# Kernel tuning notes

Hardware: AMD Instinct MI355X
Metric: run time of the kernel (lower is better)

Reference implementation:

```python
import jax, jax.numpy as jnp
import numpy as np

EPS = 1e-12  # F.normalize default eps (denominator = max(norm, eps))


def setup_inputs() -> dict:
    key = jax.random.key(0)
    ks = jax.random.split(key, 8)
    B, FIN, H, W = 4, 256, 64, 64
    N_MEM, SQ = 64, 16           # sqrt_fin = fin**0.5
    POS_CH = 2                    # PosEncoding concatenates one coord channel per dim
    CIN = FIN + POS_CH
    QK = N_MEM * SQ               # 1024
    # PosEncoding buffer: normalized coordinate grid in [-1, 1], shape [2, H, W]
    ys = jnp.linspace(-1.0, 1.0, H, dtype=jnp.float32)
    xs = jnp.linspace(-1.0, 1.0, W, dtype=jnp.float32)
    gy, gx = jnp.meshgrid(ys, xs, indexing='ij')
    pos = jnp.stack([gy, gx], axis=0)
    s = 0.02
    return {
        'x':    jax.random.normal(ks[0], (B, FIN, H, W), jnp.float32),
        'pos':  pos,
        'wq':   jax.random.normal(ks[1], (QK, CIN), jnp.float32) * s,
        'bq':   jnp.zeros((QK,), jnp.float32),
        'wk':   jax.random.normal(ks[2], (QK, CIN), jnp.float32) * s,
        'bk':   jnp.zeros((QK,), jnp.float32),
        'v':    jax.random.normal(ks[3], (N_MEM, FIN), jnp.float32) * s,
        'wout': jax.random.normal(ks[4], (FIN, FIN), jnp.float32) * s,
        'bout': jnp.zeros((FIN,), jnp.float32),
    }


def reference(x, pos, wq, bq, wk, bk, v, wout, bout):
    B, C, H, W = x.shape
    S = H * W
    n_mem, fin = v.shape
    sq = wq.shape[0] // n_mem
    # PosEncoding: concat coordinate channels
    posb = jnp.broadcast_to(pos[None], (B,) + pos.shape)
    xp = jnp.concatenate([x, posb], axis=1).reshape(B, C + pos.shape[0], S)
    # 1x1 conv projections (channel GEMMs)
    q = jnp.einsum('oc,bcs->bos', wq, xp) + bq[None, :, None]  # [B, n_mem*sq, S]
    k = jnp.einsum('oc,bcs->bos', wk, xp) + bk[None, :, None]
    q = q.reshape(B, n_mem, sq, S).transpose(0, 3, 1, 2)  # [B,S,m,sq]
    k = k.reshape(B, n_mem, sq, S).transpose(0, 3, 2, 1)  # [B,S,sq,m]
    # F.normalize: q over last dim (sqrt_fin), k over dim=1 (sqrt_fin)
    qn = q / jnp.maximum(jnp.linalg.norm(q, axis=-1, keepdims=True), EPS)
    kn = k / jnp.maximum(jnp.linalg.norm(k, axis=2, keepdims=True), EPS)
    # attn[b,s,m,n] = qn . kn ; dropout is identity in eval mode.
    # mean over memory slots m commutes with (attn @ v), so fuse:
    attn_mean = jnp.einsum('bsk,bskn->bsn', qn.mean(axis=2), kn)  # [B,S,n_mem]
    mem = attn_mean @ v                                            # [B,S,fin]
    mem = mem.transpose(0, 2, 1).reshape(B, fin, H, W)
    out = jnp.einsum('of,bfhw->bohw', wout, mem) + bout[None, :, None, None]
    return x + out
```

## Files before the change

kernel.cpp:

```cpp
#include <hip/hip_runtime.h>
#include <stdint.h>

#define EPSN 1e-12f

typedef float f32x4 __attribute__((ext_vector_type(4)));
typedef __bf16 bf16x8 __attribute__((ext_vector_type(8)));

__device__ __forceinline__ unsigned short f2bf(float f) {
  union { float f; unsigned int u; } v; v.f = f;
  unsigned int u = v.u + 0x7FFFu + ((v.u >> 16) & 1u);
  return (unsigned short)(u >> 16);
}

#define WQP_OFF 0
#define WKP_OFF (1024 * 288)
#define WVP_OFF (2 * 1024 * 288)

__global__ __launch_bounds__(256) void prep_kernel(
    const float* __restrict__ wq, const float* __restrict__ bq,
    const float* __restrict__ wk, const float* __restrict__ bk,
    const float* __restrict__ v, const float* __restrict__ wout,
    unsigned short* __restrict__ wsp) {
  int idx = blockIdx.x * 256 + threadIdx.x;
  if (idx < 1024 * 288) {
    int o = idx / 288, k = idx - o * 288;
    float vq, vk;
    if (k < 258)      { vq = wq[o * 258 + k]; vk = wk[o * 258 + k]; }
    else if (k == 258){ vq = bq[o];           vk = bk[o]; }
    else              { vq = 0.f;             vk = 0.f; }
    wsp[WQP_OFF + idx] = f2bf(vq);
    wsp[WKP_OFF + idx] = f2bf(vk);
  }
  if (idx < 256 * 64) {
    int o = idx >> 6, m = idx & 63;
    const float* wo = wout + o * 256;
    const float* vm = v + m * 256;
    float s = 0.f;
    for (int f = 0; f < 256; ++f) s = fmaf(wo[f], vm[f], s);
    wsp[WVP_OFF + idx] = f2bf(s);
  }
}

#define KP 296

__global__ __launch_bounds__(1024) void fused_kernel(
    const float* __restrict__ x, const float* __restrict__ pos,
    const unsigned short* __restrict__ wsp, const float* __restrict__ bout,
    float* __restrict__ out) {
  __shared__ __align__(16) unsigned short xp[64 * KP];
  __shared__ __align__(16) float qbarL[16 * 66];
  __shared__ __align__(16) unsigned short attnT[64 * 72];
  __shared__ float boutL[256];

  const int tid = threadIdx.x;
  const int lane = tid & 63;
  const int wid = __builtin_amdgcn_readfirstlane(tid >> 6);
  const int col = lane & 15, quad = lane >> 4;
  const int P0 = blockIdx.x * 64;
  const int b = P0 >> 12, s0 = P0 & 4095;

  for (int i = tid; i < 64 * KP; i += 1024) {
    int c = i >> 6, p = i & 63;
    float vv;
    if (c < 256)        vv = x[(b * 256 + c) * 4096 + s0 + p];
    else if (c < 258)   vv = pos[(c - 256) * 4096 + s0 + p];
    else if (c == 258)  vv = 1.0f;
    else                vv = 0.0f;
    xp[p * KP + c] = f2bf(vv);
  }
  if (tid < 256) boutL[tid] = bout[tid];
  for (int i = tid; i < 16 * 66; i += 1024) qbarL[i] = 0.f;
  __syncthreads();

  f32x4 acc[4][4];
#pragma unroll
  for (int ot = 0; ot < 4; ++ot)
#pragma unroll
    for (int nt = 0; nt < 4; ++nt) acc[ot][nt] = (f32x4)0.f;

  {
    const unsigned short* wbase = wsp + WQP_OFF + (wid * 64 + col) * 288 + quad * 8;
#pragma unroll 1
    for (int ks = 0; ks < 9; ++ks) {
      const int kb = ks * 32;
      bf16x8 av[4], bv[4];
#pragma unroll
      for (int ot = 0; ot < 4; ++ot)
        av[ot] = *(const bf16x8*)(wbase + ot * 16 * 288 + kb);
#pragma unroll
      for (int nt = 0; nt < 4; ++nt)
        bv[nt] = *(const bf16x8*)(&xp[(nt * 16 + col) * KP + kb + quad * 8]);
#pragma unroll
      for (int ot = 0; ot < 4; ++ot)
#pragma unroll
        for (int nt = 0; nt < 4; ++nt)
          acc[ot][nt] = __builtin_amdgcn_mfma_f32_16x16x32_bf16(av[ot], bv[nt], acc[ot][nt], 0, 0, 0);
    }
  }

  {
    float qsum[4][4];
#pragma unroll
    for (int nt = 0; nt < 4; ++nt)
#pragma unroll
      for (int r = 0; r < 4; ++r) qsum[nt][r] = 0.f;
#pragma unroll
    for (int ot = 0; ot < 4; ++ot) {
#pragma unroll
      for (int nt = 0; nt < 4; ++nt) {
        f32x4 a = acc[ot][nt];
        float s = a[0]*a[0] + a[1]*a[1] + a[2]*a[2] + a[3]*a[3];
        s += __shfl_xor(s, 16, 64);
        s += __shfl_xor(s, 32, 64);
        float inv = 1.0f / fmaxf(sqrtf(s), EPSN);
#pragma unroll
        for (int r = 0; r < 4; ++r) qsum[nt][r] = fmaf(a[r], inv, qsum[nt][r]);
      }
    }
#pragma unroll
    for (int nt = 0; nt < 4; ++nt)
#pragma unroll
      for (int r = 0; r < 4; ++r)
        atomicAdd(&qbarL[(quad * 4 + r) * 66 + nt * 16 + col], qsum[nt][r] * (1.0f / 64.0f));
  }
  __syncthreads();

#pragma unroll
  for (int ot = 0; ot < 4; ++ot)
#pragma unroll
    for (int nt = 0; nt < 4; ++nt) acc[ot][nt] = (f32x4)0.f;

  {
    const unsigned short* wbase = wsp + WKP_OFF + (wid * 64 + col) * 288 + quad * 8;
#pragma unroll 1
    for (int ks = 0; ks < 9; ++ks) {
      const int kb = ks * 32;
      bf16x8 av[4], bv[4];
#pragma unroll
      for (int ot = 0; ot < 4; ++ot)
        av[ot] = *(const bf16x8*)(wbase + ot * 16 * 288 + kb);
#pragma unroll
      for (int nt = 0; nt < 4; ++nt)
        bv[nt] = *(const bf16x8*)(&xp[(nt * 16 + col) * KP + kb + quad * 8]);
#pragma unroll
      for (int ot = 0; ot < 4; ++ot)
#pragma unroll
        for (int nt = 0; nt < 4; ++nt)
          acc[ot][nt] = __builtin_amdgcn_mfma_f32_16x16x32_bf16(av[ot], bv[nt], acc[ot][nt], 0, 0, 0);
    }
  }

  {
    float qb[4][4];
#pragma unroll
    for (int nt = 0; nt < 4; ++nt)
#pragma unroll
      for (int r = 0; r < 4; ++r)
        qb[nt][r] = qbarL[(quad * 4 + r) * 66 + nt * 16 + col];

#pragma unroll
    for (int ot = 0; ot < 4; ++ot) {
      const int m = wid * 4 + ot;
#pragma unroll
      for (int nt = 0; nt < 4; ++nt) {
        f32x4 a = acc[ot][nt];
        float s2 = a[0]*a[0] + a[1]*a[1] + a[2]*a[2] + a[3]*a[3];
        float sp = qb[nt][0]*a[0] + qb[nt][1]*a[1] + qb[nt][2]*a[2] + qb[nt][3]*a[3];
        s2 += __shfl_xor(s2, 16, 64);
        s2 += __shfl_xor(s2, 32, 64);
        sp += __shfl_xor(sp, 16, 64);
        sp += __shfl_xor(sp, 32, 64);
        float attn = sp / fmaxf(sqrtf(s2), EPSN);
        if (quad == 0) attnT[(nt * 16 + col) * 72 + m] = f2bf(attn);
      }
    }
  }
  __syncthreads();

  {
    f32x4 e[4];
#pragma unroll
    for (int nt = 0; nt < 4; ++nt) e[nt] = (f32x4)0.f;
    const unsigned short* wvb = wsp + WVP_OFF + (wid * 16 + col) * 64 + quad * 8;
#pragma unroll
    for (int ks = 0; ks < 2; ++ks) {
      bf16x8 av = *(const bf16x8*)(wvb + ks * 32);
#pragma unroll
      for (int nt = 0; nt < 4; ++nt) {
        bf16x8 bv = *(const bf16x8*)(&attnT[(nt * 16 + col) * 72 + ks * 32 + quad * 8]);
        e[nt] = __builtin_amdgcn_mfma_f32_16x16x32_bf16(av, bv, e[nt], 0, 0, 0);
      }
    }
#pragma unroll
    for (int nt = 0; nt < 4; ++nt) {
#pragma unroll
      for (int r = 0; r < 4; ++r) {
        const int o = wid * 16 + quad * 4 + r;
        const int p = nt * 16 + col;
        const int gi = (b * 256 + o) * 4096 + s0 + p;
        out[gi] = x[gi] + boutL[o] + e[nt][r];
      }
    }
  }
}

extern "C" void kernel_launch(void* const* d_in, const int* in_sizes, int n_in,
                              void* d_out, int out_size, void* d_ws, size_t ws_size,
                              hipStream_t stream) {
  const float* x    = (const float*)d_in[0];
  const float* pos  = (const float*)d_in[1];
  const float* wq   = (const float*)d_in[2];
  const float* bq   = (const float*)d_in[3];
  const float* wk   = (const float*)d_in[4];
  const float* bk   = (const float*)d_in[5];
  const float* v    = (const float*)d_in[6];
  const float* wout = (const float*)d_in[7];
  const float* bout = (const float*)d_in[8];
  float* out = (float*)d_out;
  unsigned short* wsp = (unsigned short*)d_ws;

  hipLaunchKernelGGL(prep_kernel, dim3(1152), dim3(256), 0, stream,
                     wq, bq, wk, bk, v, wout, wsp);
  hipLaunchKernelGGL(fused_kernel, dim3(256), dim3(1024), 0, stream,
                     x, pos, wsp, bout, out);
}
```

Baseline: 150.5 us.

## Pre-swizzle Q/K weights into MFMA fragment order and vectorize prep and staging

The prep kernel now writes the Q and K weights in MFMA fragment order, so each lane's 8-element bf16 A-operand sits contiguous and the wave's loads coalesce into one 1KB block. The K-loop over the weights is fully unrolled. The Wout·V product is split four ways per output with shuffle reduction and vector loads. The x-to-LDS staging packs two bf16 channels per 32-bit store. Together these target the strided global weight loads, the slow serial prep dot-products, and LDS store count, at the cost of more register pressure from unrolling.

```diff
diff --git a/kernel.cpp b/kernel.cpp
--- a/kernel.cpp
+++ b/kernel.cpp
@@ -5,6 +5,7 @@
 
 typedef float f32x4 __attribute__((ext_vector_type(4)));
 typedef __bf16 bf16x8 __attribute__((ext_vector_type(8)));
+typedef uint32_t u32x4 __attribute__((ext_vector_type(4)));
 
 __device__ __forceinline__ unsigned short f2bf(float f) {
   union { float f; unsigned int u; } v; v.f = f;
@@ -12,43 +13,61 @@
   return (unsigned short)(u >> 16);
 }
 
-#define WQP_OFF 0
-#define WKP_OFF (1024 * 288)
-#define WVP_OFF (2 * 1024 * 288)
+#define WQF_OFF 0
+#define WKF_OFF (64 * 9 * 64 * 8)
+#define WVP_OFF (2 * 64 * 9 * 64 * 8)
 
 __global__ __launch_bounds__(256) void prep_kernel(
     const float* __restrict__ wq, const float* __restrict__ bq,
     const float* __restrict__ wk, const float* __restrict__ bk,
     const float* __restrict__ v, const float* __restrict__ wout,
     unsigned short* __restrict__ wsp) {
-  int idx = blockIdx.x * 256 + threadIdx.x;
-  if (idx < 1024 * 288) {
-    int o = idx / 288, k = idx - o * 288;
-    float vq, vk;
-    if (k < 258)      { vq = wq[o * 258 + k]; vk = wk[o * 258 + k]; }
-    else if (k == 258){ vq = bq[o];           vk = bk[o]; }
-    else              { vq = 0.f;             vk = 0.f; }
-    wsp[WQP_OFF + idx] = f2bf(vq);
-    wsp[WKP_OFF + idx] = f2bf(vk);
-  }
-  if (idx < 256 * 64) {
-    int o = idx >> 6, m = idx & 63;
-    const float* wo = wout + o * 256;
-    const float* vm = v + m * 256;
+  if (blockIdx.x < 144) {
+    int t = blockIdx.x * 256 + threadIdx.x;
+    int lane = t & 63;
+    int rest = t >> 6;
+    int ks = rest % 9, g = rest / 9;
+    int col = lane & 15, quad = lane >> 4;
+    int o = g * 16 + col;
+    int kb = ks * 32 + quad * 8;
+    unsigned short q8[8], k8[8];
+#pragma unroll
+    for (int j = 0; j < 8; ++j) {
+      int k = kb + j;
+      float vq, vk;
+      if (k < 258)       { vq = wq[o * 258 + k]; vk = wk[o * 258 + k]; }
+      else if (k == 258) { vq = bq[o];           vk = bk[o]; }
+      else               { vq = 0.f;             vk = 0.f; }
+      q8[j] = f2bf(vq); k8[j] = f2bf(vk);
+    }
+    *(u32x4*)(wsp + WQF_OFF + t * 8) = *(u32x4*)q8;
+    *(u32x4*)(wsp + WKF_OFF + t * 8) = *(u32x4*)k8;
+  } else {
+    int idx2 = (blockIdx.x - 144) * 256 + threadIdx.x;
+    int fc = idx2 & 3, m = (idx2 >> 2) & 63, o = idx2 >> 8;
+    const f32x4* wo = (const f32x4*)(wout + o * 256 + fc * 64);
+    const f32x4* vm = (const f32x4*)(v + m * 256 + fc * 64);
     float s = 0.f;
-    for (int f = 0; f < 256; ++f) s = fmaf(wo[f], vm[f], s);
-    wsp[WVP_OFF + idx] = f2bf(s);
+#pragma unroll
+    for (int f = 0; f < 16; ++f) {
+      f32x4 a = wo[f], bvv = vm[f];
+      s += a[0]*bvv[0] + a[1]*bvv[1] + a[2]*bvv[2] + a[3]*bvv[3];
+    }
+    s += __shfl_xor(s, 1, 64);
+    s += __shfl_xor(s, 2, 64);
+    if (fc == 0) wsp[WVP_OFF + o * 64 + m] = f2bf(s);
   }
 }
 
 #define KP 296
+#define QS 66
 
 __global__ __launch_bounds__(1024) void fused_kernel(
     const float* __restrict__ x, const float* __restrict__ pos,
     const unsigned short* __restrict__ wsp, const float* __restrict__ bout,
     float* __restrict__ out) {
   __shared__ __align__(16) unsigned short xp[64 * KP];
-  __shared__ __align__(16) float qbarL[16 * 66];
+  __shared__ __align__(16) float qbarL[16 * QS];
   __shared__ __align__(16) unsigned short attnT[64 * 72];
   __shared__ float boutL[256];
 
@@ -59,19 +78,34 @@
   const int P0 = blockIdx.x * 64;
   const int b = P0 >> 12, s0 = P0 & 4095;
 
-  for (int i = tid; i < 64 * KP; i += 1024) {
-    int c = i >> 6, p = i & 63;
-    float vv;
-    if (c < 256)        vv = x[(b * 256 + c) * 4096 + s0 + p];
-    else if (c < 258)   vv = pos[(c - 256) * 4096 + s0 + p];
-    else if (c == 258)  vv = 1.0f;
-    else                vv = 0.0f;
-    xp[p * KP + c] = f2bf(vv);
+  uint32_t* xp32 = (uint32_t*)xp;
+  for (int i = tid; i < 64 * 152; i += 1024) {
+    int dc = i & 7, pp = (i >> 3) & 63, dh = i >> 9;
+    int dcol = dh * 8 + dc;
+    if (dcol < 148) {
+      int c0 = dcol * 2;
+      float v0, v1;
+      if (c0 < 256) {
+        v0 = x[(b * 256 + c0) * 4096 + s0 + pp];
+        v1 = x[(b * 256 + c0 + 1) * 4096 + s0 + pp];
+      } else if (c0 == 256) {
+        v0 = pos[s0 + pp];
+        v1 = pos[4096 + s0 + pp];
+      } else {
+        v0 = (c0 == 258) ? 1.0f : 0.0f;
+        v1 = 0.0f;
+      }
+      xp32[pp * 148 + dcol] =
+          (uint32_t)f2bf(v0) | ((uint32_t)f2bf(v1) << 16);
+    }
   }
   if (tid < 256) boutL[tid] = bout[tid];
-  for (int i = tid; i < 16 * 66; i += 1024) qbarL[i] = 0.f;
+  for (int i = tid; i < 16 * QS; i += 1024) qbarL[i] = 0.f;
   __syncthreads();
 
+  const unsigned short* aqbase = wsp + WQF_OFF + (wid * 4 * 9 * 64 + lane) * 8;
+  const unsigned short* akbase = wsp + WKF_OFF + (wid * 4 * 9 * 64 + lane) * 8;
+
   f32x4 acc[4][4];
 #pragma unroll
   for (int ot = 0; ot < 4; ++ot)
@@ -79,14 +113,13 @@
     for (int nt = 0; nt < 4; ++nt) acc[ot][nt] = (f32x4)0.f;
 
   {
-    const unsigned short* wbase = wsp + WQP_OFF + (wid * 64 + col) * 288 + quad * 8;
-#pragma unroll 1
+#pragma unroll
     for (int ks = 0; ks < 9; ++ks) {
       const int kb = ks * 32;
       bf16x8 av[4], bv[4];
 #pragma unroll
       for (int ot = 0; ot < 4; ++ot)
-        av[ot] = *(const bf16x8*)(wbase + ot * 16 * 288 + kb);
+        av[ot] = *(const bf16x8*)(aqbase + (ot * 9 + ks) * 512);
 #pragma unroll
       for (int nt = 0; nt < 4; ++nt)
         bv[nt] = *(const bf16x8*)(&xp[(nt * 16 + col) * KP + kb + quad * 8]);
@@ -121,7 +154,7 @@
     for (int nt = 0; nt < 4; ++nt)
 #pragma unroll
       for (int r = 0; r < 4; ++r)
-        atomicAdd(&qbarL[(quad * 4 + r) * 66 + nt * 16 + col], qsum[nt][r] * (1.0f / 64.0f));
+        atomicAdd(&qbarL[(quad * 4 + r) * QS + nt * 16 + col], qsum[nt][r] * (1.0f / 64.0f));
   }
   __syncthreads();
 
@@ -131,14 +164,13 @@
     for (int nt = 0; nt < 4; ++nt) acc[ot][nt] = (f32x4)0.f;
 
   {
-    const unsigned short* wbase = wsp + WKP_OFF + (wid * 64 + col) * 288 + quad * 8;
-#pragma unroll 1
+#pragma unroll
     for (int ks = 0; ks < 9; ++ks) {
       const int kb = ks * 32;
       bf16x8 av[4], bv[4];
 #pragma unroll
       for (int ot = 0; ot < 4; ++ot)
-        av[ot] = *(const bf16x8*)(wbase + ot * 16 * 288 + kb);
+        av[ot] = *(const bf16x8*)(akbase + (ot * 9 + ks) * 512);
 #pragma unroll
       for (int nt = 0; nt < 4; ++nt)
         bv[nt] = *(const bf16x8*)(&xp[(nt * 16 + col) * KP + kb + quad * 8]);
@@ -156,7 +188,7 @@
     for (int nt = 0; nt < 4; ++nt)
 #pragma unroll
       for (int r = 0; r < 4; ++r)
-        qb[nt][r] = qbarL[(quad * 4 + r) * 66 + nt * 16 + col];
+        qb[nt][r] = qbarL[(quad * 4 + r) * QS + nt * 16 + col];
 
 #pragma unroll
     for (int ot = 0; ot < 4; ++ot) {
@@ -219,7 +251,7 @@
   float* out = (float*)d_out;
   unsigned short* wsp = (unsigned short*)d_ws;
 
-  hipLaunchKernelGGL(prep_kernel, dim3(1152), dim3(256), 0, stream,
+  hipLaunchKernelGGL(prep_kernel, dim3(400), dim3(256), 0, stream,
                      wq, bq, wk, bk, v, wout, wsp);
   hipLaunchKernelGGL(fused_kernel, dim3(256), dim3(1024), 0, stream,
                      x, pos, wsp, bout, out);
```

Measured after the change: 140.3 us. -6.8%, faster.
